# Performance work log

Measured on AMD Instinct MI355X. Metric: run time of the kernel, lower is better.

## Reference

```python
import jax, jax.numpy as jnp
import numpy as np

B, N, DIM = 2, 2048, 512
H, DH = 8, 64            # heads, dim_head; inner_dim = H*DH = 512 == DIM -> to_out is Identity
BAND = 128               # mask keeps -128 <= j-i <= 127
LN_EPS = 1e-5


def _band_mask(n):
    i = jnp.arange(n)
    d = i[None, :] - i[:, None]          # j - i
    return (d >= -BAND) & (d < BAND)     # [n, n] bool


def setup_inputs() -> dict:
    key = jax.random.key(0)
    k1, k2 = jax.random.split(key, 2)
    x = jax.random.normal(k1, (B, N, DIM), dtype=jnp.float32)
    w_qkv = jax.random.normal(k2, (DIM, 3 * H * DH), dtype=jnp.float32) * (DIM ** -0.5)
    gamma = jnp.ones((DIM,), dtype=jnp.float32)
    beta = jnp.zeros((DIM,), dtype=jnp.float32)
    return {"x": x, "w_qkv": w_qkv, "gamma": gamma, "beta": beta}


def reference(x, w_qkv, gamma, beta):
    # LayerNorm
    mu = jnp.mean(x, axis=-1, keepdims=True)
    var = jnp.mean((x - mu) ** 2, axis=-1, keepdims=True)
    xn = (x - mu) * jax.lax.rsqrt(var + LN_EPS) * gamma + beta

    # qkv projection (no bias); split and reshape to [B, H, N, DH]
    qkv = xn @ w_qkv                                   # [B, N, 3*H*DH]
    q, k, v = jnp.split(qkv, 3, axis=-1)
    to_heads = lambda t: t.reshape(B, N, H, DH).transpose(0, 2, 1, 3)
    q, k, v = to_heads(q), to_heads(k), to_heads(v)

    # NOTE: original forward never applies self.scale -> no scaling here (faithful).
    attn = jnp.einsum('bhnd,bhmd->bhnm', q, k)         # [B, H, N, N]
    attn = jnp.where(_band_mask(N), attn, jnp.float32(-10000.0))
    probs = jax.nn.softmax(attn, axis=-1)
    out = jnp.einsum('bhnm,bhmd->bhnd', probs, v)      # [B, H, N, DH]
    out = out.transpose(0, 2, 1, 3).reshape(B, N, H * DH)
    return out  # to_out is Identity since inner_dim == dim
```

## Files before the change

kernel.cpp:

```cpp
#include <hip/hip_runtime.h>
#include <hip/hip_bf16.h>

#define B_    2
#define N_    2048
#define DIM_  512
#define H_    8
#define DH_   64
#define QKVW  1536
#define BAND_ 128
#define LN_EPS 1e-5f

typedef __attribute__((ext_vector_type(8))) short bf16x8;
typedef __attribute__((ext_vector_type(4))) float f32x4;
typedef __attribute__((ext_vector_type(8))) unsigned short ushort8;

__device__ __forceinline__ float bf2f(unsigned short u) {
    union { unsigned int i; float f; } w; w.i = ((unsigned int)u) << 16; return w.f;
}
__device__ __forceinline__ unsigned short f2bf(float f) {
    __hip_bfloat16 h = __float2bfloat16(f);
    return *reinterpret_cast<unsigned short*>(&h);
}
__device__ __forceinline__ void async_copy16(void* lds, const void* g) {
    __builtin_amdgcn_global_load_lds(
        (const __attribute__((address_space(1))) unsigned int*)g,
        (__attribute__((address_space(3))) unsigned int*)lds, 16, 0, 0);
}

__global__ __launch_bounds__(256) void prep_kernel(const float* __restrict__ x,
                                                   const float* __restrict__ gamma,
                                                   const float* __restrict__ beta,
                                                   const float* __restrict__ W,
                                                   unsigned short* __restrict__ xh,
                                                   unsigned short* __restrict__ xl,
                                                   unsigned short* __restrict__ Bh,
                                                   unsigned short* __restrict__ Bl) {
    __shared__ float T[64][65];
    if (blockIdx.x < 1024) {
        const int row  = blockIdx.x * 4 + (threadIdx.x >> 6);
        const int lane = threadIdx.x & 63;
        const float* xr = x + (size_t)row * DIM_ + lane * 8;
        float4 a = *(const float4*)xr;
        float4 c = *(const float4*)(xr + 4);
        float s  = (a.x + a.y) + (a.z + a.w) + (c.x + c.y) + (c.z + c.w);
        float sq = a.x*a.x + a.y*a.y + a.z*a.z + a.w*a.w
                 + c.x*c.x + c.y*c.y + c.z*c.z + c.w*c.w;
        #pragma unroll
        for (int o = 32; o; o >>= 1) { s += __shfl_xor(s, o); sq += __shfl_xor(sq, o); }
        const float mu  = s * (1.0f / DIM_);
        const float var = sq * (1.0f / DIM_) - mu * mu;
        const float rs  = rsqrtf(var + LN_EPS);
        float4 g0 = *(const float4*)(gamma + lane * 8);
        float4 g1 = *(const float4*)(gamma + lane * 8 + 4);
        float4 b0 = *(const float4*)(beta  + lane * 8);
        float4 b1 = *(const float4*)(beta  + lane * 8 + 4);
        const float fv[8] = {
            (a.x - mu) * rs * g0.x + b0.x, (a.y - mu) * rs * g0.y + b0.y,
            (a.z - mu) * rs * g0.z + b0.z, (a.w - mu) * rs * g0.w + b0.w,
            (c.x - mu) * rs * g1.x + b1.x, (c.y - mu) * rs * g1.y + b1.y,
            (c.z - mu) * rs * g1.z + b1.z, (c.w - mu) * rs * g1.w + b1.w };
        ushort8 h, l;
        #pragma unroll
        for (int j = 0; j < 8; ++j) {
            const unsigned short hv = f2bf(fv[j]);
            h[j] = hv; l[j] = f2bf(fv[j] - bf2f(hv));
        }
        *(ushort8*)(xh + (size_t)row * DIM_ + lane * 8) = h;
        *(ushort8*)(xl + (size_t)row * DIM_ + lane * 8) = l;
    } else {
        const int bx = blockIdx.x - 1024;
        const int n0 = (bx % 24) * 64, k0 = (bx / 24) * 64;
        const int tid = threadIdx.x;
        #pragma unroll
        for (int e = 0; e < 4; ++e) {
            const int lin = e * 256 + tid;
            const int kk = lin >> 4;
            const int n4 = (lin & 15) * 4;
            float4 f = *(const float4*)(W + (size_t)(k0 + kk) * QKVW + n0 + n4);
            T[kk][n4 + 0] = f.x; T[kk][n4 + 1] = f.y;
            T[kk][n4 + 2] = f.z; T[kk][n4 + 3] = f.w;
        }
        __syncthreads();
        #pragma unroll
        for (int e = 0; e < 4; ++e) {
            const int lin = e * 256 + tid;
            const int nn = lin >> 4;
            const int kq = (lin & 15) * 4;
            ushort4 h, l;
            float f;
            f = T[kq + 0][nn]; h.x = f2bf(f); l.x = f2bf(f - bf2f(h.x));
            f = T[kq + 1][nn]; h.y = f2bf(f); l.y = f2bf(f - bf2f(h.y));
            f = T[kq + 2][nn]; h.z = f2bf(f); l.z = f2bf(f - bf2f(h.z));
            f = T[kq + 3][nn]; h.w = f2bf(f); l.w = f2bf(f - bf2f(h.w));
            *(ushort4*)(Bh + (size_t)(n0 + nn) * DIM_ + k0 + kq) = h;
            *(ushort4*)(Bl + (size_t)(n0 + nn) * DIM_ + k0 + kq) = l;
        }
    }
}

__global__ __launch_bounds__(256) void gemm_mfma(const unsigned short* __restrict__ Ah,
                                                 const unsigned short* __restrict__ Al,
                                                 const unsigned short* __restrict__ Bh,
                                                 const unsigned short* __restrict__ Bl,
                                                 unsigned short* __restrict__ Qh,
                                                 unsigned short* __restrict__ Ql,
                                                 unsigned short* __restrict__ Kh,
                                                 unsigned short* __restrict__ Kl,
                                                 unsigned short* __restrict__ Vt) {
    __shared__ __attribute__((aligned(16))) unsigned short sAh[64 * 32],  sAl[64 * 32];
    __shared__ __attribute__((aligned(16))) unsigned short sBh[128 * 32], sBl[128 * 32];
    const int tid  = threadIdx.x;
    const int lane = tid & 63, wave = tid >> 6;
    const int wr = wave >> 1, wc = wave & 1;
    const int lg = lane >> 4, l16 = lane & 15;
    const int row0 = blockIdx.y * 64;
    const int col0 = blockIdx.x * 128;
    const int part = col0 >> 9;

    f32x4 acc[2][4] = {};

    for (int k0 = 0; k0 < DIM_; k0 += 32) {
        __syncthreads();
        {
            const int s0  = wave * 64;
            const int idx = s0 + lane;
            const int r   = idx >> 2;
            const int k8  = (idx & 3) * 8;
            const size_t ga = (size_t)(row0 + r) * DIM_ + k0 + k8;
            async_copy16(&sAh[s0 * 8], Ah + ga);
            if (part < 2) async_copy16(&sAl[s0 * 8], Al + ga);
        }
        #pragma unroll
        for (int e = 0; e < 2; ++e) {
            const int s0  = e * 256 + wave * 64;
            const int idx = s0 + lane;
            const int r   = idx >> 2;
            const int k8  = (idx & 3) * 8;
            const size_t gb = (size_t)(col0 + r) * DIM_ + k0 + k8;
            async_copy16(&sBh[s0 * 8], Bh + gb);
            if (part < 2) async_copy16(&sBl[s0 * 8], Bl + gb);
        }
        __syncthreads();

        const int kb = lg * 8;
        bf16x8 ah[2], bh[4];
        #pragma unroll
        for (int mi = 0; mi < 2; ++mi)
            ah[mi] = *(const bf16x8*)&sAh[(wr * 32 + mi * 16 + l16) * 32 + kb];
        #pragma unroll
        for (int ni = 0; ni < 4; ++ni)
            bh[ni] = *(const bf16x8*)&sBh[(wc * 64 + ni * 16 + l16) * 32 + kb];
        if (part < 2) {
            bf16x8 al[2], bl[4];
            #pragma unroll
            for (int mi = 0; mi < 2; ++mi)
                al[mi] = *(const bf16x8*)&sAl[(wr * 32 + mi * 16 + l16) * 32 + kb];
            #pragma unroll
            for (int ni = 0; ni < 4; ++ni)
                bl[ni] = *(const bf16x8*)&sBl[(wc * 64 + ni * 16 + l16) * 32 + kb];
            #pragma unroll
            for (int mi = 0; mi < 2; ++mi)
                #pragma unroll
                for (int ni = 0; ni < 4; ++ni) {
                    acc[mi][ni] = __builtin_amdgcn_mfma_f32_16x16x32_bf16(ah[mi], bh[ni], acc[mi][ni], 0, 0, 0);
                    acc[mi][ni] = __builtin_amdgcn_mfma_f32_16x16x32_bf16(al[mi], bh[ni], acc[mi][ni], 0, 0, 0);
                    acc[mi][ni] = __builtin_amdgcn_mfma_f32_16x16x32_bf16(ah[mi], bl[ni], acc[mi][ni], 0, 0, 0);
                }
        } else {
            #pragma unroll
            for (int mi = 0; mi < 2; ++mi)
                #pragma unroll
                for (int ni = 0; ni < 4; ++ni)
                    acc[mi][ni] = __builtin_amdgcn_mfma_f32_16x16x32_bf16(ah[mi], bh[ni], acc[mi][ni], 0, 0, 0);
        }
    }

    const int colbase = col0 + wc * 64;
    const int head = (colbase & 511) >> 6;
    if (part < 2) {
        unsigned short* __restrict__ Ih = (part == 0) ? Qh : Kh;
        unsigned short* __restrict__ Il = (part == 0) ? Ql : Kl;
        #pragma unroll
        for (int mi = 0; mi < 2; ++mi) {
            const int rb = row0 + wr * 32 + mi * 16 + lg * 4;
            const int n  = rb & 2047;
            const size_t tbase = ((size_t)((rb >> 11) * H_ + head) * 32 + (n >> 6)) * 4096;
            #pragma unroll
            for (int ni = 0; ni < 4; ++ni) {
                const int d  = ni * 16 + l16;
                const int k8 = d >> 3;
                #pragma unroll
                for (int rr = 0; rr < 4; ++rr) {
                    const int r = (n & 63) + rr;
                    const size_t off = tbase + r * 64 + ((k8 ^ (r & 7)) * 8) + (d & 7);
                    const float v = acc[mi][ni][rr];
                    const unsigned short hv = f2bf(v);
                    Ih[off] = hv;
                    Il[off] = f2bf(v - bf2f(hv));
                }
            }
        }
    } else {
        #pragma unroll
        for (int mi = 0; mi < 2; ++mi) {
            const int rb = row0 + wr * 32 + mi * 16 + lg * 4;
            const int n  = rb & 2047;
            const size_t cbase = ((size_t)((rb >> 11) * H_ + head) * 32 + (n >> 6)) * 4096;
            const int nr = n & 63;
            #pragma unroll
            for (int ni = 0; ni < 4; ++ni) {
                const int d = ni * 16 + l16;
                const size_t off = cbase + d * 64 + (((nr >> 3) ^ (d & 7)) * 8) + (nr & 7);
                ushort4 pk;
                pk.x = f2bf(acc[mi][ni][0]); pk.y = f2bf(acc[mi][ni][1]);
                pk.z = f2bf(acc[mi][ni][2]); pk.w = f2bf(acc[mi][ni][3]);
                *(ushort4*)&Vt[off] = pk;
            }
        }
    }
}

__global__ __launch_bounds__(256) void attn_mfma(const unsigned short* __restrict__ Qh,
                                                 const unsigned short* __restrict__ Ql,
                                                 const unsigned short* __restrict__ Kh,
                                                 const unsigned short* __restrict__ Kl,
                                                 const unsigned short* __restrict__ Vt,
                                                 float* __restrict__ out) {
    const int tile = blockIdx.x, h = blockIdx.y, b = blockIdx.z;
    const int i0   = tile * 64;
    const int tid  = threadIdx.x;
    const int lane = tid & 63, wave = tid >> 6;
    const int lg   = lane >> 4, l16 = lane & 15;

    __shared__ __attribute__((aligned(16))) unsigned short sKh[4096], sKl[4096], sVt[4096];
    __shared__ __attribute__((aligned(16))) unsigned short sP[4][1024];

    const size_t hb = (size_t)(b * H_ + h) * 32;

    bf16x8 qh[2], ql[2];
    {
        const int r = wave * 16 + l16;
        const size_t tb = (hb + tile) * 4096;
        #pragma unroll
        for (int kh = 0; kh < 2; ++kh) {
            const size_t off = tb + r * 64 + (((kh * 4 + lg) ^ (r & 7)) * 8);
            qh[kh] = *(const bf16x8*)(Qh + off);
            ql[kh] = *(const bf16x8*)(Ql + off);
        }
    }

    float m_run[4], l_run[4];
    f32x4 oacc[4] = {};
    #pragma unroll
    for (int r = 0; r < 4; ++r) { m_run[r] = -1e30f; l_run[r] = 0.0f; }

    #pragma unroll 1
    for (int c = 0; c < 5; ++c) {
        const int jbase = i0 - 128 + c * 64;
        if (jbase + 64 <= 0 || jbase >= N_) continue;
        __syncthreads();
        const size_t kbG = (hb + (jbase >> 6)) * 4096;
        #pragma unroll
        for (int e = 0; e < 6; ++e) {
            const int s0  = e * 256 + wave * 64;
            const int arr = s0 >> 9;
            const int w0  = (s0 & 511) * 8;
            unsigned short* dst = (arr == 0) ? sKh : (arr == 1) ? sKl : sVt;
            const unsigned short* src = (arr == 0) ? Kh : (arr == 1) ? Kl : Vt;
            async_copy16(dst + w0, src + kbG + w0 + lane * 8);
        }
        __syncthreads();

        f32x4 sacc[4] = {};
        #pragma unroll
        for (int kh = 0; kh < 2; ++kh) {
            #pragma unroll
            for (int t = 0; t < 4; ++t) {
                const int r = t * 16 + l16;
                const int off = r * 64 + ((((kh * 4 + lg)) ^ (r & 7)) * 8);
                const bf16x8 kbh = *(const bf16x8*)&sKh[off];
                const bf16x8 kbl = *(const bf16x8*)&sKl[off];
                sacc[t] = __builtin_amdgcn_mfma_f32_16x16x32_bf16(qh[kh], kbh, sacc[t], 0, 0, 0);
                sacc[t] = __builtin_amdgcn_mfma_f32_16x16x32_bf16(ql[kh], kbh, sacc[t], 0, 0, 0);
                sacc[t] = __builtin_amdgcn_mfma_f32_16x16x32_bf16(qh[kh], kbl, sacc[t], 0, 0, 0);
            }
        }

        #pragma unroll
        for (int r = 0; r < 4; ++r) {
            const int i = i0 + wave * 16 + lg * 4 + r;
            float sv[4];
            float mx = -1e30f;
            #pragma unroll
            for (int t = 0; t < 4; ++t) {
                const int j = jbase + t * 16 + l16;
                const int d = j - i;
                const bool ok = (d >= -BAND_) && (d < BAND_);
                sv[t] = ok ? sacc[t][r] : -1e30f;
                mx = fmaxf(mx, sv[t]);
            }
            #pragma unroll
            for (int o = 1; o < 16; o <<= 1) mx = fmaxf(mx, __shfl_xor(mx, o));
            const float m_new = fmaxf(m_run[r], mx);
            const float alpha = __expf(m_run[r] - m_new);
            float p[4], lc = 0.f;
            #pragma unroll
            for (int t = 0; t < 4; ++t) { p[t] = __expf(sv[t] - m_new); lc += p[t]; }
            #pragma unroll
            for (int o = 1; o < 16; o <<= 1) lc += __shfl_xor(lc, o);
            l_run[r] = l_run[r] * alpha + lc;
            m_run[r] = m_new;
            #pragma unroll
            for (int dt = 0; dt < 4; ++dt) oacc[dt][r] *= alpha;
            const int q = lg * 4 + r;
            #pragma unroll
            for (int t = 0; t < 4; ++t) {
                const int k = t * 16 + l16;
                sP[wave][q * 64 + (((k >> 3) ^ (q & 7)) * 8) + (k & 7)] = f2bf(p[t]);
            }
        }

        #pragma unroll
        for (int kh = 0; kh < 2; ++kh) {
            const int poff = l16 * 64 + ((((kh * 4 + lg)) ^ (l16 & 7)) * 8);
            const bf16x8 pa = *(const bf16x8*)&sP[wave][poff];
            #pragma unroll
            for (int dt = 0; dt < 4; ++dt) {
                const int rv = dt * 16 + l16;
                const int voff = rv * 64 + ((((kh * 4 + lg)) ^ (rv & 7)) * 8);
                const bf16x8 vb = *(const bf16x8*)&sVt[voff];
                oacc[dt] = __builtin_amdgcn_mfma_f32_16x16x32_bf16(pa, vb, oacc[dt], 0, 0, 0);
            }
        }
    }

    #pragma unroll
    for (int dt = 0; dt < 4; ++dt)
        #pragma unroll
        for (int r = 0; r < 4; ++r) {
            const int i = i0 + wave * 16 + lg * 4 + r;
            out[((size_t)b * N_ + i) * DIM_ + h * DH_ + dt * 16 + l16] = oacc[dt][r] / l_run[r];
        }
}

extern "C" void kernel_launch(void* const* d_in, const int* in_sizes, int n_in,
                              void* d_out, int out_size, void* d_ws, size_t ws_size,
                              hipStream_t stream) {
    const float* x     = (const float*)d_in[0];
    const float* w     = (const float*)d_in[1];
    const float* gamma = (const float*)d_in[2];
    const float* beta  = (const float*)d_in[3];
    float* out = (float*)d_out;

    const size_t NTOK = (size_t)B_ * N_;
    const size_t IMG  = (size_t)B_ * H_ * 32 * 4096;

    unsigned short* xnh = (unsigned short*)d_ws;
    unsigned short* xnl = xnh + NTOK * DIM_;
    unsigned short* wth = xnl + NTOK * DIM_;
    unsigned short* wtl = wth + (size_t)QKVW * DIM_;
    unsigned short* Qh  = wtl + (size_t)QKVW * DIM_;
    unsigned short* Ql  = Qh + IMG;
    unsigned short* Kh  = Ql + IMG;
    unsigned short* Kl  = Kh + IMG;
    unsigned short* Vt  = Kl + IMG;

    prep_kernel<<<dim3(1024 + 192), dim3(256), 0, stream>>>(x, gamma, beta, w, xnh, xnl, wth, wtl);
    gemm_mfma<<<dim3(QKVW / 128, (B_ * N_) / 64), dim3(256), 0, stream>>>(
        xnh, xnl, wth, wtl, Qh, Ql, Kh, Kl, Vt);
    attn_mfma<<<dim3(N_ / 64, H_, B_), dim3(256), 0, stream>>>(Qh, Ql, Kh, Kl, Vt, out);
}
```

Baseline: 52.99 us.

## Double GEMM K-step with swizzled LDS and remap blocks for XCD locality

The QKV GEMM now stages 64-wide K slices instead of 32, halving the number of barrier-separated load phases. LDS rows are XOR-swizzled to avoid bank conflicts at the wider stride. Both the GEMM and attention grids are flattened to 1D, and block IDs are remapped so consecutive tiles land on the same XCD (bid&7 selects the chiplet), which should improve L2 reuse of shared A/B rows and K/V tiles. The trade-off is doubled LDS use per block, which may lower occupancy.

New measurement: 47.08 us. 1.13x faster.

```diff
diff --git a/kernel.cpp b/kernel.cpp
--- a/kernel.cpp
+++ b/kernel.cpp
@@ -107,71 +107,87 @@
                                                  unsigned short* __restrict__ Kh,
                                                  unsigned short* __restrict__ Kl,
                                                  unsigned short* __restrict__ Vt) {
-    __shared__ __attribute__((aligned(16))) unsigned short sAh[64 * 32],  sAl[64 * 32];
-    __shared__ __attribute__((aligned(16))) unsigned short sBh[128 * 32], sBl[128 * 32];
+    __shared__ __attribute__((aligned(16))) unsigned short sAh[64 * 64],  sAl[64 * 64];
+    __shared__ __attribute__((aligned(16))) unsigned short sBh[128 * 64], sBl[128 * 64];
     const int tid  = threadIdx.x;
     const int lane = tid & 63, wave = tid >> 6;
     const int wr = wave >> 1, wc = wave & 1;
     const int lg = lane >> 4, l16 = lane & 15;
-    const int row0 = blockIdx.y * 64;
-    const int col0 = blockIdx.x * 128;
+
+    const int bid = blockIdx.x;
+    const int sb  = (bid & 7) * 96 + (bid >> 3);
+    const int row0 = (sb / 12) * 64;
+    const int col0 = (sb % 12) * 128;
     const int part = col0 >> 9;
 
     f32x4 acc[2][4] = {};
 
-    for (int k0 = 0; k0 < DIM_; k0 += 32) {
-        __syncthreads();
-        {
-            const int s0  = wave * 64;
-            const int idx = s0 + lane;
-            const int r   = idx >> 2;
-            const int k8  = (idx & 3) * 8;
-            const size_t ga = (size_t)(row0 + r) * DIM_ + k0 + k8;
-            async_copy16(&sAh[s0 * 8], Ah + ga);
-            if (part < 2) async_copy16(&sAl[s0 * 8], Al + ga);
-        }
+    for (int k0 = 0; k0 < DIM_; k0 += 64) {
+        __syncthreads();
         #pragma unroll
         for (int e = 0; e < 2; ++e) {
             const int s0  = e * 256 + wave * 64;
             const int idx = s0 + lane;
-            const int r   = idx >> 2;
-            const int k8  = (idx & 3) * 8;
-            const size_t gb = (size_t)(col0 + r) * DIM_ + k0 + k8;
+            const int r   = idx >> 3;
+            const int pb  = idx & 7;
+            const int klog = pb ^ (r & 7);
+            const size_t ga = (size_t)(row0 + r) * DIM_ + k0 + klog * 8;
+            async_copy16(&sAh[s0 * 8], Ah + ga);
+            if (part < 2) async_copy16(&sAl[s0 * 8], Al + ga);
+        }
+        #pragma unroll
+        for (int e = 0; e < 4; ++e) {
+            const int s0  = e * 256 + wave * 64;
+            const int idx = s0 + lane;
+            const int r   = idx >> 3;
+            const int pb  = idx & 7;
+            const int klog = pb ^ (r & 7);
+            const size_t gb = (size_t)(col0 + r) * DIM_ + k0 + klog * 8;
             async_copy16(&sBh[s0 * 8], Bh + gb);
             if (part < 2) async_copy16(&sBl[s0 * 8], Bl + gb);
         }
         __syncthreads();
 
-        const int kb = lg * 8;
-        bf16x8 ah[2], bh[4];
-        #pragma unroll
-        for (int mi = 0; mi < 2; ++mi)
-            ah[mi] = *(const bf16x8*)&sAh[(wr * 32 + mi * 16 + l16) * 32 + kb];
-        #pragma unroll
-        for (int ni = 0; ni < 4; ++ni)
-            bh[ni] = *(const bf16x8*)&sBh[(wc * 64 + ni * 16 + l16) * 32 + kb];
-        if (part < 2) {
-            bf16x8 al[2], bl[4];
-            #pragma unroll
-            for (int mi = 0; mi < 2; ++mi)
-                al[mi] = *(const bf16x8*)&sAl[(wr * 32 + mi * 16 + l16) * 32 + kb];
-            #pragma unroll
-            for (int ni = 0; ni < 4; ++ni)
-                bl[ni] = *(const bf16x8*)&sBl[(wc * 64 + ni * 16 + l16) * 32 + kb];
-            #pragma unroll
-            for (int mi = 0; mi < 2; ++mi)
+        #pragma unroll
+        for (int kh = 0; kh < 2; ++kh) {
+            bf16x8 ah[2], bh[4];
+            #pragma unroll
+            for (int mi = 0; mi < 2; ++mi) {
+                const int r = wr * 32 + mi * 16 + l16;
+                ah[mi] = *(const bf16x8*)&sAh[r * 64 + (((kh * 4 + lg) ^ (r & 7)) * 8)];
+            }
+            #pragma unroll
+            for (int ni = 0; ni < 4; ++ni) {
+                const int r = wc * 64 + ni * 16 + l16;
+                bh[ni] = *(const bf16x8*)&sBh[r * 64 + (((kh * 4 + lg) ^ (r & 7)) * 8)];
+            }
+            if (part < 2) {
+                bf16x8 al[2], bl[4];
+                #pragma unroll
+                for (int mi = 0; mi < 2; ++mi) {
+                    const int r = wr * 32 + mi * 16 + l16;
+                    al[mi] = *(const bf16x8*)&sAl[r * 64 + (((kh * 4 + lg) ^ (r & 7)) * 8)];
+                }
                 #pragma unroll
                 for (int ni = 0; ni < 4; ++ni) {
-                    acc[mi][ni] = __builtin_amdgcn_mfma_f32_16x16x32_bf16(ah[mi], bh[ni], acc[mi][ni], 0, 0, 0);
-                    acc[mi][ni] = __builtin_amdgcn_mfma_f32_16x16x32_bf16(al[mi], bh[ni], acc[mi][ni], 0, 0, 0);
-                    acc[mi][ni] = __builtin_amdgcn_mfma_f32_16x16x32_bf16(ah[mi], bl[ni], acc[mi][ni], 0, 0, 0);
+                    const int r = wc * 64 + ni * 16 + l16;
+                    bl[ni] = *(const bf16x8*)&sBl[r * 64 + (((kh * 4 + lg) ^ (r & 7)) * 8)];
                 }
-        } else {
-            #pragma unroll
-            for (int mi = 0; mi < 2; ++mi)
-                #pragma unroll
-                for (int ni = 0; ni < 4; ++ni)
-                    acc[mi][ni] = __builtin_amdgcn_mfma_f32_16x16x32_bf16(ah[mi], bh[ni], acc[mi][ni], 0, 0, 0);
+                #pragma unroll
+                for (int mi = 0; mi < 2; ++mi)
+                    #pragma unroll
+                    for (int ni = 0; ni < 4; ++ni) {
+                        acc[mi][ni] = __builtin_amdgcn_mfma_f32_16x16x32_bf16(ah[mi], bh[ni], acc[mi][ni], 0, 0, 0);
+                        acc[mi][ni] = __builtin_amdgcn_mfma_f32_16x16x32_bf16(al[mi], bh[ni], acc[mi][ni], 0, 0, 0);
+                        acc[mi][ni] = __builtin_amdgcn_mfma_f32_16x16x32_bf16(ah[mi], bl[ni], acc[mi][ni], 0, 0, 0);
+                    }
+            } else {
+                #pragma unroll
+                for (int mi = 0; mi < 2; ++mi)
+                    #pragma unroll
+                    for (int ni = 0; ni < 4; ++ni)
+                        acc[mi][ni] = __builtin_amdgcn_mfma_f32_16x16x32_bf16(ah[mi], bh[ni], acc[mi][ni], 0, 0, 0);
+            }
         }
     }
 
@@ -226,7 +242,11 @@
                                                  const unsigned short* __restrict__ Kl,
                                                  const unsigned short* __restrict__ Vt,
                                                  float* __restrict__ out) {
-    const int tile = blockIdx.x, h = blockIdx.y, b = blockIdx.z;
+    const int bid = blockIdx.x;
+    const int sb  = (bid & 7) * 64 + (bid >> 3);
+    const int tile = sb & 31;
+    const int h    = (sb >> 5) & 7;
+    const int b    = sb >> 8;
     const int i0   = tile * 64;
     const int tid  = threadIdx.x;
     const int lane = tid & 63, wave = tid >> 6;
@@ -366,7 +386,7 @@
     unsigned short* Vt  = Kl + IMG;
 
     prep_kernel<<<dim3(1024 + 192), dim3(256), 0, stream>>>(x, gamma, beta, w, xnh, xnl, wth, wtl);
-    gemm_mfma<<<dim3(QKVW / 128, (B_ * N_) / 64), dim3(256), 0, stream>>>(
+    gemm_mfma<<<dim3(768), dim3(256), 0, stream>>>(
         xnh, xnl, wth, wtl, Qh, Ql, Kh, Kl, Vt);
-    attn_mfma<<<dim3(N_ / 64, H_, B_), dim3(256), 0, stream>>>(Qh, Ql, Kh, Kl, Vt, out);
-}
+    attn_mfma<<<dim3(512), dim3(256), 0, stream>>>(Qh, Ql, Kh, Kl, Vt, out);
+}
```
